# Kernel tuning notes

Hardware: AMD Instinct MI355X
Metric: run time of the kernel (lower is better)

The kernel has to match this reference:

```python
import jax, jax.numpy as jnp
import numpy as np

N_NODES = 100000
N_EDGES = 3200000
IN_CH = 128
HID = 128
N_CLASSES = 32
N_GRAPHS = 256


def gcn_conv(x, W, b, src, dst, n_nodes):
    """PyG GCNConv: add self-loops, symmetric deg^-1/2 normalization,
    linear transform, gather-scatter aggregation, bias."""
    xw = x @ W  # [N, out]
    loop = jnp.arange(n_nodes, dtype=src.dtype)
    s = jnp.concatenate([src, loop])  # sources incl. self-loops
    d = jnp.concatenate([dst, loop])  # targets incl. self-loops
    deg = jax.ops.segment_sum(jnp.ones_like(d, dtype=xw.dtype), d,
                              num_segments=n_nodes)
    dinv = jnp.where(deg > 0, jax.lax.rsqrt(deg), 0.0)
    norm = dinv[s] * dinv[d]  # [E+N]
    msgs = xw[s] * norm[:, None]  # gather + scale
    out = jax.ops.segment_sum(msgs, d, num_segments=n_nodes)  # scatter-add
    return out + b


def global_mean_pool(x, batch, n_graphs):
    sums = jax.ops.segment_sum(x, batch, num_segments=n_graphs)
    cnt = jax.ops.segment_sum(jnp.ones((x.shape[0],), x.dtype), batch,
                              num_segments=n_graphs)
    return sums / jnp.maximum(cnt, 1.0)[:, None]


def setup_inputs() -> dict:
    key = jax.random.key(0)
    ks = jax.random.split(key, 9)
    x = jax.random.normal(ks[0], (N_NODES, IN_CH), dtype=jnp.float32)
    edge_index = jax.random.randint(ks[1], (2, N_EDGES), 0, N_NODES, dtype=jnp.int32)
    batch = jnp.sort(jax.random.randint(ks[2], (N_NODES,), 0, N_GRAPHS, dtype=jnp.int32))
    s1 = 1.0 / np.sqrt(IN_CH)
    s2 = 1.0 / np.sqrt(HID)
    W1 = jax.random.uniform(ks[3], (IN_CH, HID), jnp.float32, -s1, s1)
    b1 = jnp.zeros((HID,), jnp.float32)
    W2 = jax.random.uniform(ks[4], (HID, HID), jnp.float32, -s2, s2)
    b2 = jnp.zeros((HID,), jnp.float32)
    Wfc = jax.random.uniform(ks[5], (HID, N_CLASSES), jnp.float32, -s2, s2)
    bfc = jax.random.uniform(ks[6], (N_CLASSES,), jnp.float32, -s2, s2)
    return {"x": x, "edge_index": edge_index, "batch": batch,
            "W1": W1, "b1": b1, "W2": W2, "b2": b2, "Wfc": Wfc, "bfc": bfc}


def reference(x, edge_index, batch, W1, b1, W2, b2, Wfc, bfc):
    src, dst = edge_index[0], edge_index[1]
    h = jax.nn.relu(gcn_conv(x, W1, b1, src, dst, N_NODES))
    h = jax.nn.relu(gcn_conv(h, W2, b2, src, dst, N_NODES))
    g = global_mean_pool(h, batch, N_GRAPHS)  # [G, HID]
    return g @ Wfc + bfc  # [G, N_CLASSES]
```

## Files before the change

kernel.cpp:

```cpp
#include <hip/hip_runtime.h>
#include <hip/hip_bf16.h>
#include <hip/hip_fp16.h>

static constexpr int CH     = 128;
static constexpr int NCLS   = 32;
static constexpr int NGRAPH = 256;

static constexpr int BSHIFT = 8;
static constexpr int BW     = 1 << BSHIFT;
static constexpr int MAXB   = 512;

typedef _Float16 half8 __attribute__((ext_vector_type(8)));
typedef _Float16 half4 __attribute__((ext_vector_type(4)));
typedef float    f32x4 __attribute__((ext_vector_type(4)));
typedef float    f32x2 __attribute__((ext_vector_type(2)));

static constexpr float FP8_SCALE = 64.0f;
static constexpr float FP8_INV   = 1.0f / 64.0f;

__device__ __forceinline__ unsigned char enc8(float v) {
  return (unsigned char)(__builtin_amdgcn_cvt_pk_fp8_f32(v, v, 0, false) & 0xFF);
}

__global__ __launch_bounds__(1024) void k_scatter(
    const int* __restrict__ src, const int* __restrict__ dst,
    int* __restrict__ gcur, int* __restrict__ ebuf, int E, int CAP,
    int* __restrict__ xzero, const int* __restrict__ batch,
    int* __restrict__ gstart, int* __restrict__ gend, int Nn) {
  __shared__ int bcnt[MAXB];
  __shared__ int lofs[MAXB];
  __shared__ int bbase[MAXB];
  __shared__ int sorted[8192];
  __shared__ unsigned short sbkt[8192];
  int t = threadIdx.x;
  if (blockIdx.x == 0 && t < 32) xzero[t] = 0;
  {
    int i = blockIdx.x * 1024 + t;
    if (i < Nn) {
      int bg = batch[i];
      if (i == 0 || batch[i - 1] != bg) gstart[bg] = i;
      if (i == Nn - 1 || batch[i + 1] != bg) gend[bg] = i + 1;
    }
  }
  if (t < MAXB) bcnt[t] = 0;
  __syncthreads();
  int base = blockIdx.x * 8192;
  int cnt = E - base; if (cnt > 8192) cnt = 8192;
  int p_[8], b_[8], r_[8];
  #pragma unroll
  for (int j = 0; j < 8; ++j) {
    int i = j * 1024 + t;
    if (i < cnt) {
      int s = src[base + i], d = dst[base + i];
      b_[j] = d >> BSHIFT;
      p_[j] = ((d & (BW - 1)) << 17) | s;
      r_[j] = atomicAdd(&bcnt[b_[j]], 1);
    }
  }
  __syncthreads();
  if (t < MAXB) lofs[t] = bcnt[t];
  __syncthreads();
  for (int st = 1; st < MAXB; st <<= 1) {
    int v = (t < MAXB && t >= st) ? lofs[t - st] : 0;
    __syncthreads();
    if (t < MAXB) lofs[t] += v;
    __syncthreads();
  }
  if (t < MAXB && bcnt[t]) bbase[t] = atomicAdd(&gcur[t], bcnt[t]);
  __syncthreads();
  #pragma unroll
  for (int j = 0; j < 8; ++j) {
    int i = j * 1024 + t;
    if (i < cnt) {
      int pos = lofs[b_[j]] - bcnt[b_[j]] + r_[j];
      sorted[pos] = p_[j];
      sbkt[pos] = (unsigned short)b_[j];
    }
  }
  __syncthreads();
  for (int i = t; i < cnt; i += 1024) {
    int bk = sbkt[i];
    ebuf[bk * CAP + bbase[bk] + (i - (lofs[bk] - bcnt[bk]))] = sorted[i];
  }
}

__global__ __launch_bounds__(1024) void k_build(
    const int* __restrict__ ebuf, const int* __restrict__ gcur,
    int* __restrict__ offs, int* __restrict__ oend,
    float* __restrict__ dinv, int* __restrict__ csr, int N, int CAP,
    const float* __restrict__ W1, const float* __restrict__ W2,
    _Float16* __restrict__ WhT1, _Float16* __restrict__ WhT2) {
  __shared__ int sdeg[BW];
  __shared__ int sscan[BW];
  __shared__ int cur[BW];
  __shared__ int chist[BW];
  __shared__ int clofs[BW];
  __shared__ int lsorted[8192];
  __shared__ unsigned char lnode[8192];
  int b = blockIdx.x;
  int t = threadIdx.x;

  int gi = b * 1024 + t;
  if (gi < 2 * CH * CH) {
    const float* W = (gi < CH * CH) ? W1 : W2;
    _Float16* T   = (gi < CH * CH) ? WhT1 : WhT2;
    int j = gi & (CH * CH - 1);
    int k = j >> 7, n = j & 127;
    T[n * CH + k] = (_Float16)W[j];
  }

  int lo = b << BSHIFT;
  int e0 = b * CAP;
  int CNT = gcur[b];

  if (t < BW) sdeg[t] = 0;
  __syncthreads();
  for (int i = t; i < CNT; i += 1024)
    atomicAdd(&sdeg[ebuf[e0 + i] >> 17], 1);
  __syncthreads();
  if (t < BW) sscan[t] = (sdeg[t] + 3) & ~3;
  __syncthreads();
  for (int st = 1; st < BW; st <<= 1) {
    int v = (t < BW && t >= st) ? sscan[t - st] : 0;
    __syncthreads();
    if (t < BW) sscan[t] += v;
    __syncthreads();
  }
  if (t < BW) {
    int deg  = sdeg[t];
    int pdeg = (deg + 3) & ~3;
    int ex = b * CAP + sscan[t] - pdeg;
    int n = lo + t;
    if (n < N) {
      offs[n] = ex;
      oend[n] = ex + deg;
      dinv[n] = 1.0f / sqrtf((float)(deg + 1));
      for (int q = deg; q < pdeg; ++q) csr[ex + q] = N;
      cur[t] = ex;
    }
  }
  __syncthreads();

  for (int c0 = 0; c0 < CNT; c0 += 8192) {
    int ccnt = CNT - c0; if (ccnt > 8192) ccnt = 8192;
    if (t < BW) chist[t] = 0;
    __syncthreads();
    int p_[8], nd_[8], r_[8];
    #pragma unroll
    for (int j = 0; j < 8; ++j) {
      int i = j * 1024 + t;
      if (i < ccnt) {
        p_[j] = ebuf[e0 + c0 + i];
        nd_[j] = p_[j] >> 17;
        r_[j] = atomicAdd(&chist[nd_[j]], 1);
      }
    }
    __syncthreads();
    if (t < BW) clofs[t] = chist[t];
    __syncthreads();
    for (int st = 1; st < BW; st <<= 1) {
      int v = (t < BW && t >= st) ? clofs[t - st] : 0;
      __syncthreads();
      if (t < BW) clofs[t] += v;
      __syncthreads();
    }
    #pragma unroll
    for (int j = 0; j < 8; ++j) {
      int i = j * 1024 + t;
      if (i < ccnt) {
        int pos = clofs[nd_[j]] - chist[nd_[j]] + r_[j];
        lsorted[pos] = p_[j];
        lnode[pos] = (unsigned char)nd_[j];
      }
    }
    __syncthreads();
    for (int i = t; i < ccnt; i += 1024) {
      int nd = lnode[i];
      int gpos = cur[nd] + (i - (clofs[nd] - chist[nd]));
      csr[gpos] = lsorted[i] & 0x1FFFF;
    }
    __syncthreads();
    if (t < BW) cur[t] += chist[t];
    __syncthreads();
  }
}

__device__ __forceinline__ void stage_w(const _Float16* __restrict__ WhT,
                                        _Float16 (*Ws)[136], int tid) {
  #pragma unroll
  for (int l = 0; l < 8; ++l) {
    int idx = tid + l * 256;
    int n = idx >> 4, k8 = (idx & 15) << 3;
    *(half8*)&Ws[n][k8] = *(const half8*)(WhT + n * CH + k8);
  }
}

__device__ __forceinline__ void gemm_tile(
    const _Float16 (*Ws)[136], const half8* af,
    const float* __restrict__ dinv, unsigned char* __restrict__ C,
    int tile, int M, int quad, int sub) {
  f32x4 acc[8];
  #pragma unroll
  for (int j = 0; j < 8; ++j) acc[j] = (f32x4){0.f, 0.f, 0.f, 0.f};
  #pragma unroll
  for (int kc = 0; kc < 4; ++kc) {
    #pragma unroll
    for (int nt = 0; nt < 8; ++nt) {
      half8 b = *(const half8*)&Ws[nt * 16 + sub][kc * 32 + quad * 8];
      acc[nt] = __builtin_amdgcn_mfma_f32_16x16x32_f16(af[kc], b, acc[nt], 0, 0, 0);
    }
  }
  #pragma unroll
  for (int r = 0; r < 4; ++r) {
    int orow = tile * 16 + quad * 4 + r;
    if (orow < M) {
      float d = dinv[orow] * FP8_SCALE;
      #pragma unroll
      for (int nt = 0; nt < 8; ++nt)
        C[(size_t)orow * CH + nt * 16 + sub] = enc8(acc[nt][r] * d);
    }
  }
}

__global__ __launch_bounds__(256) void k_gemm_f32(
    const float* __restrict__ A, const _Float16* __restrict__ WhT,
    const float* __restrict__ dinv, unsigned char* __restrict__ C, int M) {
  __shared__ _Float16 Ws[128][136];
  int tid = threadIdx.x;
  stage_w(WhT, Ws, tid);
  __syncthreads();
  int lane = tid & 63;
  int quad = lane >> 4, sub = lane & 15;
  int ntiles = (M + 15) >> 4;
  int wid0 = blockIdx.x * 4 + (tid >> 6);
  int wstep = gridDim.x * 4;
  for (int tile = wid0; tile < ntiles; tile += wstep) {
    int row = tile * 16 + sub; if (row >= M) row = M - 1;
    const float* arow = A + (size_t)row * CH + quad * 8;
    half8 af[4];
    #pragma unroll
    for (int kc = 0; kc < 4; ++kc) {
      float4 v0 = *(const float4*)(arow + kc * 32);
      float4 v1 = *(const float4*)(arow + kc * 32 + 4);
      af[kc] = (half8){(_Float16)v0.x, (_Float16)v0.y, (_Float16)v0.z, (_Float16)v0.w,
                       (_Float16)v1.x, (_Float16)v1.y, (_Float16)v1.z, (_Float16)v1.w};
    }
    gemm_tile(Ws, af, dinv, C, tile, M, quad, sub);
  }
}

__global__ __launch_bounds__(256) void k_gemm_f16(
    const _Float16* __restrict__ A, const _Float16* __restrict__ WhT,
    const float* __restrict__ dinv, unsigned char* __restrict__ C, int M) {
  __shared__ _Float16 Ws[128][136];
  int tid = threadIdx.x;
  stage_w(WhT, Ws, tid);
  __syncthreads();
  int lane = tid & 63;
  int quad = lane >> 4, sub = lane & 15;
  int ntiles = (M + 15) >> 4;
  int wid0 = blockIdx.x * 4 + (tid >> 6);
  int wstep = gridDim.x * 4;
  for (int tile = wid0; tile < ntiles; tile += wstep) {
    int row = tile * 16 + sub; if (row >= M) row = M - 1;
    const _Float16* arow = A + (size_t)row * CH + quad * 8;
    half8 af[4];
    #pragma unroll
    for (int kc = 0; kc < 4; ++kc)
      af[kc] = *(const half8*)(arow + kc * 32);
    gemm_tile(Ws, af, dinv, C, tile, M, quad, sub);
  }
}

__global__ __launch_bounds__(256) void k_agg(
    const unsigned int* __restrict__ xs32, const int* __restrict__ csr,
    const int* __restrict__ offs, const int* __restrict__ oend,
    const float* __restrict__ dinv, const float* __restrict__ bias,
    __half* __restrict__ out, int N) {
  int lane  = threadIdx.x & 63;
  int wid0  = blockIdx.x * 4 + (threadIdx.x >> 6);
  int wstep = gridDim.x * 4;
  int e = lane >> 5;
  unsigned int c = lane & 31;
  float4 bb = *(const float4*)(bias + c * 4);

  auto G = [&](int s) -> unsigned int {
    return xs32[((unsigned int)s << 5) | c];
  };

  for (int wid = wid0; wid * 2 < N; wid += wstep) {
    int nA = wid * 2, nB = nA + 1;
    bool hasB = (nB < N);

    int eA = offs[nA];
    int cA = (oend[nA] - eA + 3) >> 2;
    int eB = hasB ? offs[nB] : eA;
    int cB = hasB ? ((oend[nB] - eB + 3) >> 2) : 0;

    f32x2 a0 = {0.f, 0.f}, a1 = {0.f, 0.f};
    f32x2 b0 = {0.f, 0.f}, b1 = {0.f, 0.f};
    if (e == 0) {
      unsigned int ow = G(nA);
      a0 = __builtin_amdgcn_cvt_pk_f32_fp8((int)ow, false);
      a1 = __builtin_amdgcn_cvt_pk_f32_fp8((int)ow, true);
      if (hasB) {
        unsigned int ob = G(nB);
        b0 = __builtin_amdgcn_cvt_pk_f32_fp8((int)ob, false);
        b1 = __builtin_amdgcn_cvt_pk_f32_fp8((int)ob, true);
      }
    }

    #define ACC(d, x0, x1) \
      x0 += __builtin_amdgcn_cvt_pk_f32_fp8((int)(d), false); \
      x1 += __builtin_amdgcn_cvt_pk_f32_fp8((int)(d), true);

    if (cA >= 2 && cB >= 2) {
      int4 ca0 = *(const int4*)(csr + eA);
      int4 ca1 = *(const int4*)(csr + eA + 4);
      int4 cb0 = *(const int4*)(csr + eB);
      int4 cb1 = *(const int4*)(csr + eB + 4);
      do {
        int sA0 = e ? ca0.y : ca0.x, sA1 = e ? ca0.w : ca0.z;
        int sA2 = e ? ca1.y : ca1.x, sA3 = e ? ca1.w : ca1.z;
        int sB0 = e ? cb0.y : cb0.x, sB1 = e ? cb0.w : cb0.z;
        int sB2 = e ? cb1.y : cb1.x, sB3 = e ? cb1.w : cb1.z;
        unsigned int dA0 = G(sA0), dA1 = G(sA1), dA2 = G(sA2), dA3 = G(sA3);
        unsigned int dB0 = G(sB0), dB1 = G(sB1), dB2 = G(sB2), dB3 = G(sB3);
        eA += 8; eB += 8; cA -= 2; cB -= 2;
        int4 na0 = *(const int4*)(csr + eA);
        int4 na1 = *(const int4*)(csr + eA + 4);
        int4 nb0 = *(const int4*)(csr + eB);
        int4 nb1 = *(const int4*)(csr + eB + 4);
        ACC(dA0, a0, a1); ACC(dA1, a0, a1); ACC(dA2, a0, a1); ACC(dA3, a0, a1);
        ACC(dB0, b0, b1); ACC(dB1, b0, b1); ACC(dB2, b0, b1); ACC(dB3, b0, b1);
        ca0 = na0; ca1 = na1; cb0 = nb0; cb1 = nb1;
      } while (cA >= 2 && cB >= 2);
    }

    auto drain = [&](int ee, int cc, f32x2& x0, f32x2& x1) {
      while (cc >= 2) {
        int4 q0 = *(const int4*)(csr + ee);
        int4 q1 = *(const int4*)(csr + ee + 4);
        int s0 = e ? q0.y : q0.x, s1 = e ? q0.w : q0.z;
        int s2 = e ? q1.y : q1.x, s3 = e ? q1.w : q1.z;
        unsigned int d0 = G(s0), d1 = G(s1), d2 = G(s2), d3 = G(s3);
        ACC(d0, x0, x1); ACC(d1, x0, x1); ACC(d2, x0, x1); ACC(d3, x0, x1);
        ee += 8; cc -= 2;
      }
      if (cc > 0) {
        int4 q0 = *(const int4*)(csr + ee);
        int s0 = e ? q0.y : q0.x, s1 = e ? q0.w : q0.z;
        unsigned int d0 = G(s0), d1 = G(s1);
        ACC(d0, x0, x1); ACC(d1, x0, x1);
      }
    };
    drain(eA, cA, a0, a1);
    if (hasB) drain(eB, cB, b0, b1);
    #undef ACC

    a0[0] += __shfl_xor(a0[0], 32); a0[1] += __shfl_xor(a0[1], 32);
    a1[0] += __shfl_xor(a1[0], 32); a1[1] += __shfl_xor(a1[1], 32);
    if (hasB) {
      b0[0] += __shfl_xor(b0[0], 32); b0[1] += __shfl_xor(b0[1], 32);
      b1[0] += __shfl_xor(b1[0], 32); b1[1] += __shfl_xor(b1[1], 32);
    }

    if (e == 0) {
      {
        float dn = dinv[nA] * FP8_INV;
        float r0 = fmaf(a0[0], dn, bb.x), r1 = fmaf(a0[1], dn, bb.y);
        float r2 = fmaf(a1[0], dn, bb.z), r3 = fmaf(a1[1], dn, bb.w);
        __half2 h0 = __floats2half2_rn(fmaxf(r0, 0.f), fmaxf(r1, 0.f));
        __half2 h1 = __floats2half2_rn(fmaxf(r2, 0.f), fmaxf(r3, 0.f));
        __half2* op = (__half2*)(out + (size_t)nA * CH + c * 4);
        op[0] = h0; op[1] = h1;
      }
      if (hasB) {
        float dn = dinv[nB] * FP8_INV;
        float r0 = fmaf(b0[0], dn, bb.x), r1 = fmaf(b0[1], dn, bb.y);
        float r2 = fmaf(b1[0], dn, bb.z), r3 = fmaf(b1[1], dn, bb.w);
        __half2 h0 = __floats2half2_rn(fmaxf(r0, 0.f), fmaxf(r1, 0.f));
        __half2 h1 = __floats2half2_rn(fmaxf(r2, 0.f), fmaxf(r3, 0.f));
        __half2* op = (__half2*)(out + (size_t)nB * CH + c * 4);
        op[0] = h0; op[1] = h1;
      }
    }
  }
}

__global__ __launch_bounds__(256) void k_pool(
    const __half* __restrict__ h, const int* __restrict__ batch,
    float* __restrict__ gsum, int N) {
  int t = threadIdx.x;
  int ch2 = t & 63;
  int rh  = t >> 6;
  int n0 = blockIdx.x * 64;
  int n1 = n0 + 64; if (n1 > N) n1 = N;
  int n = n0 + rh;
  if (n >= n1) return;
  const __half2* h2 = (const __half2*)h;
  int curg = batch[n];
  float ax = 0.f, ay = 0.f;
  #pragma unroll 4
  for (; n < n1; n += 4) {
    int g = batch[n];
    float2 v = __half22float2(h2[(size_t)n * 64 + ch2]);
    if (g != curg) {
      atomicAdd(&gsum[curg * CH + 2 * ch2], ax);
      atomicAdd(&gsum[curg * CH + 2 * ch2 + 1], ay);
      ax = 0.f; ay = 0.f; curg = g;
    }
    ax += v.x; ay += v.y;
  }
  atomicAdd(&gsum[curg * CH + 2 * ch2], ax);
  atomicAdd(&gsum[curg * CH + 2 * ch2 + 1], ay);
}

__global__ __launch_bounds__(256) void k_fc(
    const float* __restrict__ gsum, const int* __restrict__ gstart,
    const int* __restrict__ gend, const float* __restrict__ Wfc,
    const float* __restrict__ bfc, float* __restrict__ outp) {
  __shared__ float part[8][NCLS];
  int g = blockIdx.x;
  int t = threadIdx.x;
  int j = t & 31, seg = t >> 5;
  float acc = 0.f;
  #pragma unroll
  for (int k = 0; k < 16; ++k) {
    int cc = seg * 16 + k;
    acc = fmaf(gsum[g * CH + cc], Wfc[cc * NCLS + j], acc);
  }
  part[seg][j] = acc;
  __syncthreads();
  if (t < NCLS) {
    float s = part[0][t] + part[1][t] + part[2][t] + part[3][t]
            + part[4][t] + part[5][t] + part[6][t] + part[7][t];
    int cnt = gend[g] - gstart[g];
    float invc = 1.0f / fmaxf((float)cnt, 1.0f);
    outp[g * NCLS + t] = fmaf(s, invc, bfc[t]);
  }
}

extern "C" void kernel_launch(void* const* d_in, const int* in_sizes, int n_in,
                              void* d_out, int out_size, void* d_ws, size_t ws_size,
                              hipStream_t stream) {
  const float* x    = (const float*)d_in[0];
  const int*   ei   = (const int*)d_in[1];
  const int*   batch= (const int*)d_in[2];
  const float* W1   = (const float*)d_in[3];
  const float* b1   = (const float*)d_in[4];
  const float* W2   = (const float*)d_in[5];
  const float* b2   = (const float*)d_in[6];
  const float* Wfc  = (const float*)d_in[7];
  const float* bfc  = (const float*)d_in[8];
  float* outp = (float*)d_out;

  const int N = in_sizes[0] / CH;
  const int E = in_sizes[1] / 2;
  const int* src = ei;
  const int* dst = ei + E;
  const int NBUCK = (N + BW - 1) >> BSHIFT;
  int CAP = (E / NBUCK) + (E / NBUCK) / 8 + 1280;
  CAP = (CAP + 3) & ~3;

  char* w = (char*)d_ws;
  size_t o = 0;
  auto carve = [&](size_t bytes) -> void* {
    o = (o + 255) & ~(size_t)255;
    void* p = w + o;
    o += bytes;
    return p;
  };
  int*      gcur   = (int*)     carve(MAXB * 4);
  float*    gsum   = (float*)   carve((size_t)NGRAPH * CH * 4);
  size_t zbytes = o;
  int*      gstart = (int*)     carve((size_t)NGRAPH * 4);
  int*      gend   = (int*)     carve((size_t)NGRAPH * 4);
  int*      offs   = (int*)     carve((size_t)N * 4);
  int*      oendb  = (int*)     carve((size_t)N * 4);
  int*      csr    = (int*)     carve((size_t)NBUCK * CAP * 4);
  float*    dinv   = (float*)   carve((size_t)N * 4);
  _Float16* WhT1   = (_Float16*)carve((size_t)CH * CH * 2);
  _Float16* WhT2   = (_Float16*)carve((size_t)CH * CH * 2);
  unsigned char* xsbuf = (unsigned char*)carve((size_t)(N + 1) * CH);
  __half*   hbuf   = (__half*)  carve((size_t)N * CH * 2);
  (void)ws_size;

  int* ebuf = (int*)hbuf;

  (void)hipMemsetAsync(gcur, 0, zbytes, stream);

  const int GBW = 1024;
  const int PB  = (N + 63) / 64;
  int AB = (N + 7) / 8;
  if (AB > 2048) AB = 2048;

  k_scatter<<<(E + 8191) / 8192, 1024, 0, stream>>>(
      src, dst, gcur, ebuf, E, CAP, (int*)(xsbuf + (size_t)N * CH),
      batch, gstart, gend, N);
  k_build<<<NBUCK, 1024, 0, stream>>>(ebuf, gcur, offs, oendb, dinv, csr,
                                      N, CAP, W1, W2, WhT1, WhT2);

  k_gemm_f32<<<GBW, 256, 0, stream>>>(x, WhT1, dinv, xsbuf, N);
  k_agg<<<AB, 256, 0, stream>>>((const unsigned int*)xsbuf, csr, offs, oendb,
                                dinv, b1, hbuf, N);
  k_gemm_f16<<<GBW, 256, 0, stream>>>((const _Float16*)hbuf, WhT2, dinv, xsbuf, N);
  k_agg<<<AB, 256, 0, stream>>>((const unsigned int*)xsbuf, csr, offs, oendb,
                                dinv, b2, hbuf, N);

  k_pool<<<PB, 256, 0, stream>>>(hbuf, batch, gsum, N);
  k_fc<<<NGRAPH, 256, 0, stream>>>(gsum, gstart, gend, Wfc, bfc, outp);
  (void)out_size; (void)n_in;
}
```

Measured before the change: 300.6 us.

## Simplify CSR build: direct atomic-rank scatter and register-held single-pass bucket sort

```diff
diff --git a/kernel.cpp b/kernel.cpp
--- a/kernel.cpp
+++ b/kernel.cpp
@@ -26,16 +26,16 @@
     const int* __restrict__ src, const int* __restrict__ dst,
     int* __restrict__ gcur, int* __restrict__ ebuf, int E, int CAP,
     int* __restrict__ xzero, const int* __restrict__ batch,
-    int* __restrict__ gstart, int* __restrict__ gend, int Nn) {
+    int* __restrict__ gstart, int* __restrict__ gend,
+    float* __restrict__ gsum, int Nn) {
   __shared__ int bcnt[MAXB];
-  __shared__ int lofs[MAXB];
   __shared__ int bbase[MAXB];
-  __shared__ int sorted[8192];
-  __shared__ unsigned short sbkt[8192];
   int t = threadIdx.x;
-  if (blockIdx.x == 0 && t < 32) xzero[t] = 0;
+  int b = blockIdx.x;
+  if (b == 0 && t < 32) xzero[t] = 0;
   {
-    int i = blockIdx.x * 1024 + t;
+    int i = b * 1024 + t;
+    if (i < NGRAPH * CH) gsum[i] = 0.f;
     if (i < Nn) {
       int bg = batch[i];
       if (i == 0 || batch[i - 1] != bg) gstart[bg] = i;
@@ -44,43 +44,26 @@
   }
   if (t < MAXB) bcnt[t] = 0;
   __syncthreads();
-  int base = blockIdx.x * 8192;
-  int cnt = E - base; if (cnt > 8192) cnt = 8192;
-  int p_[8], b_[8], r_[8];
+  int base = b * 8192;
+  int p_[8], bk_[8], r_[8];
   #pragma unroll
   for (int j = 0; j < 8; ++j) {
-    int i = j * 1024 + t;
-    if (i < cnt) {
-      int s = src[base + i], d = dst[base + i];
-      b_[j] = d >> BSHIFT;
-      p_[j] = ((d & (BW - 1)) << 17) | s;
-      r_[j] = atomicAdd(&bcnt[b_[j]], 1);
-    }
-  }
-  __syncthreads();
-  if (t < MAXB) lofs[t] = bcnt[t];
-  __syncthreads();
-  for (int st = 1; st < MAXB; st <<= 1) {
-    int v = (t < MAXB && t >= st) ? lofs[t - st] : 0;
-    __syncthreads();
-    if (t < MAXB) lofs[t] += v;
-    __syncthreads();
-  }
+    int i = base + j * 1024 + t;
+    if (i < E) {
+      int s = src[i], d = dst[i];
+      bk_[j] = d >> BSHIFT;
+      p_[j]  = ((d & (BW - 1)) << 17) | s;
+      r_[j]  = atomicAdd(&bcnt[bk_[j]], 1);
+    }
+  }
+  __syncthreads();
   if (t < MAXB && bcnt[t]) bbase[t] = atomicAdd(&gcur[t], bcnt[t]);
   __syncthreads();
   #pragma unroll
   for (int j = 0; j < 8; ++j) {
-    int i = j * 1024 + t;
-    if (i < cnt) {
-      int pos = lofs[b_[j]] - bcnt[b_[j]] + r_[j];
-      sorted[pos] = p_[j];
-      sbkt[pos] = (unsigned short)b_[j];
-    }
-  }
-  __syncthreads();
-  for (int i = t; i < cnt; i += 1024) {
-    int bk = sbkt[i];
-    ebuf[bk * CAP + bbase[bk] + (i - (lofs[bk] - bcnt[bk]))] = sorted[i];
+    int i = base + j * 1024 + t;
+    if (i < E)
+      ebuf[bk_[j] * CAP + bbase[bk_[j]] + r_[j]] = p_[j];
   }
 }
 
@@ -91,12 +74,8 @@
     const float* __restrict__ W1, const float* __restrict__ W2,
     _Float16* __restrict__ WhT1, _Float16* __restrict__ WhT2) {
   __shared__ int sdeg[BW];
-  __shared__ int sscan[BW];
-  __shared__ int cur[BW];
-  __shared__ int chist[BW];
-  __shared__ int clofs[BW];
-  __shared__ int lsorted[8192];
-  __shared__ unsigned char lnode[8192];
+  __shared__ int sex[BW];
+  __shared__ int wtot[4];
   int b = blockIdx.x;
   int t = threadIdx.x;
 
@@ -115,73 +94,57 @@
 
   if (t < BW) sdeg[t] = 0;
   __syncthreads();
-  for (int i = t; i < CNT; i += 1024)
-    atomicAdd(&sdeg[ebuf[e0 + i] >> 17], 1);
-  __syncthreads();
-  if (t < BW) sscan[t] = (sdeg[t] + 3) & ~3;
-  __syncthreads();
-  for (int st = 1; st < BW; st <<= 1) {
-    int v = (t < BW && t >= st) ? sscan[t - st] : 0;
-    __syncthreads();
-    if (t < BW) sscan[t] += v;
-    __syncthreads();
-  }
+
+  constexpr int K = 11;
+  int p_[K], r_[K];
+  #pragma unroll
+  for (int k = 0; k < K; ++k) {
+    int i = k * 1024 + t;
+    if (i < CNT) {
+      p_[k] = ebuf[e0 + i];
+      r_[k] = atomicAdd(&sdeg[p_[k] >> 17], 1);
+    }
+  }
+  __syncthreads();
+
+  int lane = t & 63, wv = t >> 6;
+  int deg = 0, pdeg = 0, incl = 0;
   if (t < BW) {
-    int deg  = sdeg[t];
-    int pdeg = (deg + 3) & ~3;
-    int ex = b * CAP + sscan[t] - pdeg;
+    deg  = sdeg[t];
+    pdeg = (deg + 3) & ~3;
+    int v = pdeg;
+    #pragma unroll
+    for (int d = 1; d < 64; d <<= 1) {
+      int u = __shfl_up(v, d);
+      if (lane >= d) v += u;
+    }
+    if (lane == 63) wtot[wv] = v;
+    incl = v;
+  }
+  __syncthreads();
+  if (t < BW) {
+    int pre = 0;
+    #pragma unroll
+    for (int w2 = 0; w2 < 3; ++w2) if (w2 < wv) pre += wtot[w2];
+    int ex = e0 + (incl + pre) - pdeg;
     int n = lo + t;
     if (n < N) {
       offs[n] = ex;
       oend[n] = ex + deg;
       dinv[n] = 1.0f / sqrtf((float)(deg + 1));
       for (int q = deg; q < pdeg; ++q) csr[ex + q] = N;
-      cur[t] = ex;
-    }
-  }
-  __syncthreads();
-
-  for (int c0 = 0; c0 < CNT; c0 += 8192) {
-    int ccnt = CNT - c0; if (ccnt > 8192) ccnt = 8192;
-    if (t < BW) chist[t] = 0;
-    __syncthreads();
-    int p_[8], nd_[8], r_[8];
-    #pragma unroll
-    for (int j = 0; j < 8; ++j) {
-      int i = j * 1024 + t;
-      if (i < ccnt) {
-        p_[j] = ebuf[e0 + c0 + i];
-        nd_[j] = p_[j] >> 17;
-        r_[j] = atomicAdd(&chist[nd_[j]], 1);
-      }
-    }
-    __syncthreads();
-    if (t < BW) clofs[t] = chist[t];
-    __syncthreads();
-    for (int st = 1; st < BW; st <<= 1) {
-      int v = (t < BW && t >= st) ? clofs[t - st] : 0;
-      __syncthreads();
-      if (t < BW) clofs[t] += v;
-      __syncthreads();
-    }
-    #pragma unroll
-    for (int j = 0; j < 8; ++j) {
-      int i = j * 1024 + t;
-      if (i < ccnt) {
-        int pos = clofs[nd_[j]] - chist[nd_[j]] + r_[j];
-        lsorted[pos] = p_[j];
-        lnode[pos] = (unsigned char)nd_[j];
-      }
-    }
-    __syncthreads();
-    for (int i = t; i < ccnt; i += 1024) {
-      int nd = lnode[i];
-      int gpos = cur[nd] + (i - (clofs[nd] - chist[nd]));
-      csr[gpos] = lsorted[i] & 0x1FFFF;
-    }
-    __syncthreads();
-    if (t < BW) cur[t] += chist[t];
-    __syncthreads();
+      sex[t] = ex;
+    }
+  }
+  __syncthreads();
+
+  #pragma unroll
+  for (int k = 0; k < K; ++k) {
+    int i = k * 1024 + t;
+    if (i < CNT) {
+      int nd = p_[k] >> 17;
+      csr[sex[nd] + r_[k]] = p_[k] & 0x1FFFF;
+    }
   }
 }
 
@@ -473,7 +436,6 @@
   };
   int*      gcur   = (int*)     carve(MAXB * 4);
   float*    gsum   = (float*)   carve((size_t)NGRAPH * CH * 4);
-  size_t zbytes = o;
   int*      gstart = (int*)     carve((size_t)NGRAPH * 4);
   int*      gend   = (int*)     carve((size_t)NGRAPH * 4);
   int*      offs   = (int*)     carve((size_t)N * 4);
@@ -488,7 +450,7 @@
 
   int* ebuf = (int*)hbuf;
 
-  (void)hipMemsetAsync(gcur, 0, zbytes, stream);
+  (void)hipMemsetAsync(gcur, 0, MAXB * 4, stream);
 
   const int GBW = 1024;
   const int PB  = (N + 63) / 64;
@@ -497,7 +459,7 @@
 
   k_scatter<<<(E + 8191) / 8192, 1024, 0, stream>>>(
       src, dst, gcur, ebuf, E, CAP, (int*)(xsbuf + (size_t)N * CH),
-      batch, gstart, gend, N);
+      batch, gstart, gend, gsum, N);
   k_build<<<NBUCK, 1024, 0, stream>>>(ebuf, gcur, offs, oendb, dinv, csr,
                                       N, CAP, W1, W2, WhT1, WhT2);
 
```

After: 311.1 us. +3.5%, slower.
